# Performance work log

Hardware: AMD Instinct MI355X
Metric: run time of the kernel (lower is better)

The kernel has to match this reference:

```python
import jax, jax.numpy as jnp
import numpy as np

DIM = 1024
NUM_HEADS = 16
HEAD_DIM = DIM // NUM_HEADS
SCALE = HEAD_DIM ** (-0.5)


def setup_inputs() -> dict:
    key = jax.random.key(0)
    ks = jax.random.split(key, 10)
    b, nq, nkv = 1, 4096, 4096
    s = DIM ** -0.5
    return {
        "q": jax.random.normal(ks[0], (b, nq, DIM), jnp.float32),
        "kv": jax.random.normal(ks[1], (b, nkv, DIM), jnp.float32),
        "q_w": jax.random.normal(ks[2], (DIM, DIM), jnp.float32) * s,
        "q_b": jnp.zeros((DIM,), jnp.float32),
        "k_w": jax.random.normal(ks[3], (DIM, DIM), jnp.float32) * s,
        "k_b": jnp.zeros((DIM,), jnp.float32),
        "v_w": jax.random.normal(ks[4], (DIM, DIM), jnp.float32) * s,
        "v_b": jnp.zeros((DIM,), jnp.float32),
        "o_w": jax.random.normal(ks[5], (DIM, DIM), jnp.float32) * s,
        "o_b": jnp.zeros((DIM,), jnp.float32),
    }


def reference(q, kv, q_w, q_b, k_w, k_b, v_w, v_b, o_w, o_b):
    b, nq, _ = q.shape
    nkv = kv.shape[1]
    h, c = NUM_HEADS, HEAD_DIM
    # projections (torch Linear: x @ W^T + b); split into heads
    qh = (q @ q_w.T + q_b).reshape(b, nq, h, c).transpose(0, 2, 1, 3)   # b h nq c
    kh = (kv @ k_w.T + k_b).reshape(b, nkv, h, c).transpose(0, 2, 1, 3)  # b h nkv c
    vh = (kv @ v_w.T + v_b).reshape(b, nkv, h, c).transpose(0, 2, 1, 3)  # b h nkv c
    # full attention score matrix (non-fused, as in source)
    attn = jnp.einsum('bhqc,bhkc->bhqk', qh, kh) * SCALE
    attn = jax.nn.softmax(attn, axis=-1)
    out = jnp.einsum('bhqk,bhkc->bhqc', attn, vh)  # b h nq c
    out = out.transpose(0, 2, 1, 3).reshape(b, nq, h * c)
    out = out @ o_w.T + o_b
    return out
```

## Files before the change

### kernel.cpp

```cpp
#include <hip/hip_runtime.h>


typedef unsigned short ushort_t;
typedef unsigned short ushort4v __attribute__((ext_vector_type(4)));
typedef unsigned short ushort8 __attribute__((ext_vector_type(8)));
typedef __bf16 bf16x8 __attribute__((ext_vector_type(8)));
typedef float f32x4 __attribute__((ext_vector_type(4)));
typedef float f32x16 __attribute__((ext_vector_type(16)));
typedef unsigned int uint4v __attribute__((ext_vector_type(4)));

#define SEQ 4096
#define DIM 1024
#define NH 16
#define HD 64
#define QSCALE 0.18033688011112042f

__device__ inline ushort_t fcvt(float f) {
    return __builtin_bit_cast(ushort_t, (__bf16)f);
}
__device__ inline bf16x8 frag_of(ushort8 t) {
    return __builtin_bit_cast(bf16x8, t);
}
__device__ inline bf16x8 lds_frag(const ushort_t* p) {
    return frag_of(*(const ushort8*)p);
}
__device__ inline unsigned pk2(float a, float b) {
    return (unsigned)fcvt(a) | ((unsigned)fcvt(b) << 16);
}
__device__ inline void plswap(unsigned& a, unsigned& b) {
    asm("v_permlane32_swap_b32 %0, %1" : "+v"(a), "+v"(b));
}
__device__ inline int swz(int row, int col) {
    return row * 64 + (col ^ ((row & 7) << 3));
}
__device__ __attribute__((always_inline)) inline void gload16(
    const ushort_t* g, ushort_t* l)
{
    __builtin_amdgcn_global_load_lds(
        (const __attribute__((address_space(1))) void*)g,
        (__attribute__((address_space(3))) void*)l, 16, 0, 0);
}

__global__ __launch_bounds__(256) void cvt2(
    const float* __restrict__ s0, ushort_t* __restrict__ d0,
    const float* __restrict__ s1, ushort_t* __restrict__ d1, int n8)
{
    const float* s = blockIdx.y ? s1 : s0;
    ushort_t*    d = blockIdx.y ? d1 : d0;
    int i = blockIdx.x * 256 + threadIdx.x;
    if (i >= n8) return;
    const f32x4* sp = (const f32x4*)s + (size_t)i * 2;
    f32x4 a = sp[0], b = sp[1];
    ushort8 o;
    for (int k = 0; k < 4; ++k) { o[k] = fcvt(a[k]); o[k + 4] = fcvt(b[k]); }
    *((ushort8*)d + i) = o;
}

__global__ __launch_bounds__(256) void cvt4(
    const float* __restrict__ s0, ushort_t* __restrict__ d0,
    const float* __restrict__ s1, ushort_t* __restrict__ d1,
    const float* __restrict__ s2, ushort_t* __restrict__ d2,
    const float* __restrict__ s3, ushort_t* __restrict__ d3, int n8)
{
    const float* ss[4] = {s0, s1, s2, s3};
    ushort_t*    dd[4] = {d0, d1, d2, d3};
    const float* s = ss[blockIdx.y];
    ushort_t*    d = dd[blockIdx.y];
    int i = blockIdx.x * 256 + threadIdx.x;
    if (i >= n8) return;
    const f32x4* sp = (const f32x4*)s + (size_t)i * 2;
    f32x4 a = sp[0], b = sp[1];
    ushort8 o;
    for (int k = 0; k < 4; ++k) { o[k] = fcvt(a[k]); o[k + 4] = fcvt(b[k]); }
    *((ushort8*)d + i) = o;
}

template<int BM, int BN>
__device__ __attribute__((always_inline)) inline void gemm_core3(
    const ushort_t* __restrict__ A, const ushort_t* __restrict__ W,
    int m0, int n0, int tid, f32x4 (&acc)[BM / 32][BN / 32], ushort_t* sLDS)
{
    constexpr int TA = BM * 32;
    constexpr int TB = BN * 32;
    ushort_t* const aB0 = sLDS;
    ushort_t* const aB1 = sLDS + TA;
    ushort_t* const bB0 = sLDS + 2 * TA;
    ushort_t* const bB1 = sLDS + 2 * TA + TB;

    const int w    = tid >> 6;
    const int lane = tid & 63;
    const int quad = lane >> 4;
    const int l15  = lane & 15;
    const int wm   = w >> 1;
    const int wn   = w & 1;

    const int srow = lane >> 2;
    const int sch  = (((lane & 3) ^ ((lane >> 3) & 3)) << 3);
    const ushort_t* Ag = A + (size_t)(m0 + w * (BM / 4) + srow) * DIM + sch;
    const ushort_t* Bg = W + (size_t)(n0 + w * (BN / 4) + srow) * DIM + sch;
    const int aOff = w * (BM / 4) * 32;
    const int bOff = w * (BN / 4) * 32;

    for (int i = 0; i < BM / 64; ++i)
        gload16(Ag + (size_t)(i * 16) * DIM, aB0 + aOff + i * 512);
    for (int i = 0; i < BN / 64; ++i)
        gload16(Bg + (size_t)(i * 16) * DIM, bB0 + bOff + i * 512);
    __syncthreads();

    const int slot = (quad ^ ((l15 >> 1) & 3)) << 3;
    for (int it = 0; it < DIM / 32; ++it) {
        const int cur = it & 1;
        ushort_t* aC = cur ? aB1 : aB0;
        ushort_t* bC = cur ? bB1 : bB0;
        ushort_t* aN = cur ? aB0 : aB1;
        ushort_t* bN = cur ? bB0 : bB1;

        if (it + 1 < DIM / 32) {
            const int k0 = (it + 1) * 32;
            for (int i = 0; i < BM / 64; ++i)
                gload16(Ag + k0 + (size_t)(i * 16) * DIM, aN + aOff + i * 512);
            for (int i = 0; i < BN / 64; ++i)
                gload16(Bg + k0 + (size_t)(i * 16) * DIM, bN + bOff + i * 512);
        }

        bf16x8 af[BM / 32], bf[BN / 32];
        for (int i = 0; i < BM / 32; ++i) {
            int row = wm * (BM / 2) + i * 16 + l15;
            af[i] = lds_frag(aC + row * 32 + slot);
        }
        for (int j = 0; j < BN / 32; ++j) {
            int row = wn * (BN / 2) + j * 16 + l15;
            bf[j] = lds_frag(bC + row * 32 + slot);
        }
        for (int i = 0; i < BM / 32; ++i)
            for (int j = 0; j < BN / 32; ++j)
                acc[i][j] = __builtin_amdgcn_mfma_f32_16x16x32_bf16(
                    af[i], bf[j], acc[i][j], 0, 0, 0);
        __syncthreads();
    }
}

__global__ __launch_bounds__(256, 3) void proj3(
    const ushort_t* __restrict__ Qb, const ushort_t* __restrict__ KVb,
    const ushort_t* __restrict__ qwb, const ushort_t* __restrict__ kwb,
    const ushort_t* __restrict__ vwb,
    const float* __restrict__ q_b, const float* __restrict__ k_b,
    const float* __restrict__ v_b,
    ushort_t* __restrict__ Qp, ushort_t* __restrict__ Kp,
    ushort_t* __restrict__ VpT)
{
    __shared__ __align__(1024) ushort_t sLDS[17536];

    const int z = blockIdx.z;
    const ushort_t* A = z ? KVb : Qb;
    const ushort_t* W = (z == 0) ? qwb : (z == 1 ? kwb : vwb);
    const float* bias = (z == 0) ? q_b : (z == 1 ? k_b : v_b);
    const int tid = threadIdx.x;
    const int m0 = blockIdx.y * 128;
    const int n0 = blockIdx.x * 128;

    f32x4 acc[4][4] = {};
    gemm_core3<128, 128>(A, W, m0, n0, tid, acc, sLDS);

    const int lane = tid & 63, quad = lane >> 4, l15 = lane & 15;
    const int wm = (tid >> 6) >> 1, wn = (tid >> 6) & 1;

    if (z == 2) {
        const int TSTR = 136;
        for (int j = 0; j < 4; ++j) {
            int col = wn * 64 + j * 16 + l15;
            float bj = bias[n0 + col];
            for (int i = 0; i < 4; ++i) {
                int row = wm * 64 + i * 16 + quad * 4;
                ushort4v o4;
                for (int r = 0; r < 4; ++r) o4[r] = fcvt(acc[i][j][r] + bj);
                *(ushort4v*)(sLDS + col * TSTR + row) = o4;
            }
        }
        __syncthreads();
        const int vrow = tid >> 1;
        const int vc   = (tid & 1) * 64;
        ushort_t* dst = VpT + (size_t)(n0 + vrow) * SEQ + m0 + vc;
        const ushort_t* src = sLDS + vrow * TSTR + vc;
        for (int k = 0; k < 8; ++k)
            *(ushort8*)(dst + k * 8) = *(const ushort8*)(src + k * 8);
    } else {
        const float scale = (z == 0) ? QSCALE : 1.0f;
        ushort_t* C = z ? Kp : Qp;
        for (int j = 0; j < 4; ++j) {
            int col = n0 + wn * 64 + j * 16 + l15;
            float bj = bias[col];
            for (int i = 0; i < 4; ++i) {
                int row = m0 + wm * 64 + i * 16 + quad * 4;
                for (int r = 0; r < 4; ++r)
                    C[(size_t)(row + r) * DIM + col] =
                        fcvt((acc[i][j][r] + bj) * scale);
            }
        }
    }
}

__global__ __launch_bounds__(256, 4) void gemm_out(
    const ushort_t* __restrict__ A, const ushort_t* __restrict__ W,
    const float* __restrict__ bias, float* __restrict__ C)
{
    __shared__ __align__(1024) ushort_t sLDS[8192];

    const int tid = threadIdx.x;
    const int m0 = blockIdx.y * 64;
    const int n0 = blockIdx.x * 64;

    f32x4 acc[2][2] = {};
    gemm_core3<64, 64>(A, W, m0, n0, tid, acc, sLDS);

    const int lane = tid & 63, quad = lane >> 4, l15 = lane & 15;
    const int wm = (tid >> 6) >> 1, wn = (tid >> 6) & 1;
    for (int j = 0; j < 2; ++j) {
        int col = n0 + wn * 32 + j * 16 + l15;
        float bj = bias[col];
        for (int i = 0; i < 2; ++i) {
            int row = m0 + wm * 32 + i * 16 + quad * 4;
            for (int r = 0; r < 4; ++r)
                C[(size_t)(row + r) * DIM + col] = acc[i][j][r] + bj;
        }
    }
}

#define TILE 4096
#define BUFE (2 * TILE)
__global__ __launch_bounds__(256, 2) void attn_kernel(
    const ushort_t* __restrict__ Q, const ushort_t* __restrict__ K,
    const ushort_t* __restrict__ VT, ushort_t* __restrict__ O)
{
    __shared__ __align__(16) ushort_t sB[2 * BUFE];

    const int tid  = threadIdx.x;
    const int w    = tid >> 6;
    const int lane = tid & 63;
    const int l31  = lane & 31;
    const int hi   = lane >> 5;
    const int h    = blockIdx.x;
    const int q0   = blockIdx.y * 128 + w * 32;
    const int hHD  = h * HD;

    const int srow0 = tid >> 3;
    const int srow1 = srow0 + 32;
    const int sch   = (tid & 7) << 3;
    const ushort_t* Kg0 = K  + (size_t)srow0 * DIM + hHD + sch;
    const ushort_t* Kg1 = K  + (size_t)srow1 * DIM + hHD + sch;
    const ushort_t* Vg0 = VT + (size_t)(hHD + srow0) * SEQ + sch;
    const ushort_t* Vg1 = VT + (size_t)(hHD + srow1) * SEQ + sch;
    const int lk0 = swz(srow0, sch), lk1 = swz(srow1, sch);

    const ushort_t* qb = Q + (size_t)(q0 + l31) * DIM + hHD + hi * 8;
    bf16x8 qf[4];
    for (int ks = 0; ks < 4; ++ks)
        qf[ks] = frag_of(*(const ushort8*)(qb + ks * 16));

    bf16x8 onef;
    for (int i = 0; i < 8; ++i) onef[i] = (__bf16)1.0f;

    *(ushort8*)(sB + lk0)        = *(const ushort8*)(Kg0);
    *(ushort8*)(sB + lk1)        = *(const ushort8*)(Kg1);
    *(ushort8*)(sB + TILE + lk0) = *(const ushort8*)(Vg0);
    *(ushort8*)(sB + TILE + lk1) = *(const ushort8*)(Vg1);
    __syncthreads();

    f32x16 oacc[2] = {};
    f32x16 lacc = {};

    for (int it = 0; it < SEQ / 64; ++it) {
        const int cur = it & 1;
        const int kvn = (it + 1) * 64;
        ushort_t* bK = sB + cur * BUFE;
        ushort_t* bV = bK + TILE;

        ushort8 gk0, gk1, gv0, gv1;
        if (kvn < SEQ) {
            gk0 = *(const ushort8*)(Kg0 + (size_t)kvn * DIM);
            gk1 = *(const ushort8*)(Kg1 + (size_t)kvn * DIM);
            gv0 = *(const ushort8*)(Vg0 + kvn);
            gv1 = *(const ushort8*)(Vg1 + kvn);
        }

        bf16x8 kf[8], vf[8];
        for (int t = 0; t < 2; ++t)
            for (int ks = 0; ks < 4; ++ks) {
                int r = t * 32 + l31;
                kf[t * 4 + ks] = lds_frag(bK + swz(r, ks * 16 + hi * 8));
            }
        for (int dt = 0; dt < 2; ++dt)
            for (int ks = 0; ks < 4; ++ks) {
                int r = dt * 32 + l31;
                vf[ks * 2 + dt] = lds_frag(bV + swz(r, ks * 16 + hi * 8));
            }

        f32x16 sacc[2] = {};
        for (int t = 0; t < 2; ++t)
            for (int ks = 0; ks < 4; ++ks)
                sacc[t] = __builtin_amdgcn_mfma_f32_32x32x16_bf16(
                    kf[t * 4 + ks], qf[ks], sacc[t], 0, 0, 0);

        for (int t = 0; t < 2; ++t)
            for (int r = 0; r < 16; ++r)
                sacc[t][r] = __builtin_amdgcn_exp2f(sacc[t][r]);

        for (int ks = 0; ks < 4; ++ks) {
            const int t = ks >> 1, s8 = (ks & 1) * 8;
            unsigned p00 = pk2(sacc[t][s8 + 0], sacc[t][s8 + 1]);
            unsigned p01 = pk2(sacc[t][s8 + 2], sacc[t][s8 + 3]);
            unsigned p10 = pk2(sacc[t][s8 + 4], sacc[t][s8 + 5]);
            unsigned p11 = pk2(sacc[t][s8 + 6], sacc[t][s8 + 7]);
            plswap(p00, p10);
            plswap(p01, p11);
            uint4v wv; wv[0] = p00; wv[1] = p01; wv[2] = p10; wv[3] = p11;
            bf16x8 pf = __builtin_bit_cast(bf16x8, wv);
            for (int dt = 0; dt < 2; ++dt)
                oacc[dt] = __builtin_amdgcn_mfma_f32_32x32x16_bf16(
                    vf[ks * 2 + dt], pf, oacc[dt], 0, 0, 0);
            lacc = __builtin_amdgcn_mfma_f32_32x32x16_bf16(
                onef, pf, lacc, 0, 0, 0);
        }

        if (kvn < SEQ) {
            ushort_t* nB = sB + (cur ^ 1) * BUFE;
            *(ushort8*)(nB + lk0)        = gk0;
            *(ushort8*)(nB + lk1)        = gk1;
            *(ushort8*)(nB + TILE + lk0) = gv0;
            *(ushort8*)(nB + TILE + lk1) = gv1;
        }
        __syncthreads();
    }

    float inv = 1.f / lacc[0];
    int qrow = q0 + l31;
    for (int dt = 0; dt < 2; ++dt)
        for (int g = 0; g < 4; ++g) {
            ushort4v o4;
            for (int r = 0; r < 4; ++r) o4[r] = fcvt(oacc[dt][g * 4 + r] * inv);
            *(ushort4v*)(O + (size_t)qrow * DIM + hHD + dt * 32 + g * 8 + hi * 4) = o4;
        }
}

extern "C" void kernel_launch(void* const* d_in, const int* in_sizes, int n_in,
                              void* d_out, int out_size, void* d_ws, size_t ws_size,
                              hipStream_t stream)
{
    const float* q   = (const float*)d_in[0];
    const float* kv  = (const float*)d_in[1];
    const float* q_w = (const float*)d_in[2];
    const float* q_b = (const float*)d_in[3];
    const float* k_w = (const float*)d_in[4];
    const float* k_b = (const float*)d_in[5];
    const float* v_w = (const float*)d_in[6];
    const float* v_b = (const float*)d_in[7];
    const float* o_w = (const float*)d_in[8];
    const float* o_b = (const float*)d_in[9];
    float* out = (float*)d_out;

    const size_t SD = (size_t)SEQ * DIM;
    const size_t WW = (size_t)DIM * DIM;
    ushort_t* Qp  = (ushort_t*)d_ws;
    ushort_t* Kp  = Qp + SD;
    ushort_t* VpT = Kp + SD;
    ushort_t* AO  = VpT + SD;
    ushort_t* Qb  = AO;
    ushort_t* KVb = AO + SD;
    ushort_t* qwb = KVb + SD;
    ushort_t* kwb = qwb + WW;
    ushort_t* vwb = kwb + WW;
    ushort_t* owb = vwb + WW;

    cvt2<<<dim3((unsigned)(SD / 8 / 256), 2), 256, 0, stream>>>(
        q, Qb, kv, KVb, (int)(SD / 8));
    cvt4<<<dim3((unsigned)(WW / 8 / 256), 4), 256, 0, stream>>>(
        q_w, qwb, k_w, kwb, v_w, vwb, o_w, owb, (int)(WW / 8));

    proj3<<<dim3(DIM / 128, SEQ / 128, 3), 256, 0, stream>>>(
        Qb, KVb, qwb, kwb, vwb, q_b, k_b, v_b, Qp, Kp, VpT);
    attn_kernel<<<dim3(NH, SEQ / 128), 256, 0, stream>>>(Qp, Kp, VpT, AO);
    gemm_out<<<dim3(DIM / 64, SEQ / 64), 256, 0, stream>>>(AO, owb, o_b, out);
}
```

Measured before the change: 247.0 us.

## Remap blocks across XCDs and compute softmax row sums with VALU

All three main kernels now launch a flat 1D grid and remap block ids so that consecutive logical tiles land on the same XCD. This lets blocks that share A/W rows, or the same head's K/V, reuse that XCD's L2. The attention kernel also drops the extra MFMA against a ones vector that produced the softmax denominator. It instead sums the exponentials in registers and combines the two half-waves with a cross-lane shuffle, trading one matrix op per k-step for VALU adds and a shuffle. The sum is taken over fp32 exponentials rather than the bf16-rounded values fed to the PV product, so normalisation differs slightly.

```diff
diff --git a/kernel.cpp b/kernel.cpp
--- a/kernel.cpp
+++ b/kernel.cpp
@@ -32,6 +32,9 @@
 }
 __device__ inline int swz(int row, int col) {
     return row * 64 + (col ^ ((row & 7) << 3));
+}
+__device__ inline int xcd_swz(int bid, int nwg) {
+    return (bid & 7) * (nwg >> 3) + (bid >> 3);
 }
 __device__ __attribute__((always_inline)) inline void gload16(
     const ushort_t* g, ushort_t* l)
@@ -151,13 +154,16 @@
 {
     __shared__ __align__(1024) ushort_t sLDS[17536];
 
-    const int z = blockIdx.z;
+    const int lb = xcd_swz(blockIdx.x, 768);
+    const int z  = lb >> 8;
+    const int r  = lb & 255;
+    const int m0 = (r >> 3) * 128;
+    const int n0 = (r & 7) * 128;
+
     const ushort_t* A = z ? KVb : Qb;
     const ushort_t* W = (z == 0) ? qwb : (z == 1 ? kwb : vwb);
     const float* bias = (z == 0) ? q_b : (z == 1 ? k_b : v_b);
     const int tid = threadIdx.x;
-    const int m0 = blockIdx.y * 128;
-    const int n0 = blockIdx.x * 128;
 
     f32x4 acc[4][4] = {};
     gemm_core3<128, 128>(A, W, m0, n0, tid, acc, sLDS);
@@ -173,7 +179,7 @@
             for (int i = 0; i < 4; ++i) {
                 int row = wm * 64 + i * 16 + quad * 4;
                 ushort4v o4;
-                for (int r = 0; r < 4; ++r) o4[r] = fcvt(acc[i][j][r] + bj);
+                for (int r2 = 0; r2 < 4; ++r2) o4[r2] = fcvt(acc[i][j][r2] + bj);
                 *(ushort4v*)(sLDS + col * TSTR + row) = o4;
             }
         }
@@ -192,9 +198,9 @@
             float bj = bias[col];
             for (int i = 0; i < 4; ++i) {
                 int row = m0 + wm * 64 + i * 16 + quad * 4;
-                for (int r = 0; r < 4; ++r)
-                    C[(size_t)(row + r) * DIM + col] =
-                        fcvt((acc[i][j][r] + bj) * scale);
+                for (int r2 = 0; r2 < 4; ++r2)
+                    C[(size_t)(row + r2) * DIM + col] =
+                        fcvt((acc[i][j][r2] + bj) * scale);
             }
         }
     }
@@ -206,9 +212,10 @@
 {
     __shared__ __align__(1024) ushort_t sLDS[8192];
 
+    const int lb = xcd_swz(blockIdx.x, 1024);
+    const int m0 = (lb >> 4) * 64;
+    const int n0 = (lb & 15) * 64;
     const int tid = threadIdx.x;
-    const int m0 = blockIdx.y * 64;
-    const int n0 = blockIdx.x * 64;
 
     f32x4 acc[2][2] = {};
     gemm_core3<64, 64>(A, W, m0, n0, tid, acc, sLDS);
@@ -234,13 +241,16 @@
 {
     __shared__ __align__(16) ushort_t sB[2 * BUFE];
 
+    const int lb   = xcd_swz(blockIdx.x, 512);
+    const int h    = lb >> 5;
+    const int qblk = lb & 31;
+
     const int tid  = threadIdx.x;
     const int w    = tid >> 6;
     const int lane = tid & 63;
     const int l31  = lane & 31;
     const int hi   = lane >> 5;
-    const int h    = blockIdx.x;
-    const int q0   = blockIdx.y * 128 + w * 32;
+    const int q0   = qblk * 128 + w * 32;
     const int hHD  = h * HD;
 
     const int srow0 = tid >> 3;
@@ -257,9 +267,6 @@
     for (int ks = 0; ks < 4; ++ks)
         qf[ks] = frag_of(*(const ushort8*)(qb + ks * 16));
 
-    bf16x8 onef;
-    for (int i = 0; i < 8; ++i) onef[i] = (__bf16)1.0f;
-
     *(ushort8*)(sB + lk0)        = *(const ushort8*)(Kg0);
     *(ushort8*)(sB + lk1)        = *(const ushort8*)(Kg1);
     *(ushort8*)(sB + TILE + lk0) = *(const ushort8*)(Vg0);
@@ -267,7 +274,7 @@
     __syncthreads();
 
     f32x16 oacc[2] = {};
-    f32x16 lacc = {};
+    float l_i = 0.f;
 
     for (int it = 0; it < SEQ / 64; ++it) {
         const int cur = it & 1;
@@ -301,9 +308,14 @@
                 sacc[t] = __builtin_amdgcn_mfma_f32_32x32x16_bf16(
                     kf[t * 4 + ks], qf[ks], sacc[t], 0, 0, 0);
 
+        float lp = 0.f;
         for (int t = 0; t < 2; ++t)
-            for (int r = 0; r < 16; ++r)
-                sacc[t][r] = __builtin_amdgcn_exp2f(sacc[t][r]);
+            for (int r = 0; r < 16; ++r) {
+                float p = __builtin_amdgcn_exp2f(sacc[t][r]);
+                sacc[t][r] = p;
+                lp += p;
+            }
+        l_i += lp + __shfl_xor(lp, 32);
 
         for (int ks = 0; ks < 4; ++ks) {
             const int t = ks >> 1, s8 = (ks & 1) * 8;
@@ -318,8 +330,6 @@
             for (int dt = 0; dt < 2; ++dt)
                 oacc[dt] = __builtin_amdgcn_mfma_f32_32x32x16_bf16(
                     vf[ks * 2 + dt], pf, oacc[dt], 0, 0, 0);
-            lacc = __builtin_amdgcn_mfma_f32_32x32x16_bf16(
-                onef, pf, lacc, 0, 0, 0);
         }
 
         if (kvn < SEQ) {
@@ -332,7 +342,7 @@
         __syncthreads();
     }
 
-    float inv = 1.f / lacc[0];
+    float inv = 1.f / l_i;
     int qrow = q0 + l31;
     for (int dt = 0; dt < 2; ++dt)
         for (int g = 0; g < 4; ++g) {
@@ -376,8 +386,8 @@
     cvt4<<<dim3((unsigned)(WW / 8 / 256), 4), 256, 0, stream>>>(
         q_w, qwb, k_w, kwb, v_w, vwb, o_w, owb, (int)(WW / 8));
 
-    proj3<<<dim3(DIM / 128, SEQ / 128, 3), 256, 0, stream>>>(
+    proj3<<<dim3(768), 256, 0, stream>>>(
         Qb, KVb, qwb, kwb, vwb, q_b, k_b, v_b, Qp, Kp, VpT);
-    attn_kernel<<<dim3(NH, SEQ / 128), 256, 0, stream>>>(Qp, Kp, VpT, AO);
-    gemm_out<<<dim3(DIM / 64, SEQ / 64), 256, 0, stream>>>(AO, owb, o_b, out);
-}
+    attn_kernel<<<dim3(512), 256, 0, stream>>>(Qp, Kp, VpT, AO);
+    gemm_out<<<dim3(1024), 256, 0, stream>>>(AO, owb, o_b, out);
+}
```

Result: no change. 245.7 us (-0.5%).
